# Optimization experiments

Hardware: AMD Instinct MI355X
Metric: run time of the kernel (lower is better)

## Reference

```python
import jax, jax.numpy as jnp
import numpy as np

N = 100000   # nodes
E = 1600000  # edges (before self-loops)
D_IN = 128
HID = 64
H1 = 4       # heads of conv1
OUT = 2
EPS = 1e-5
NEG_SLOPE = 0.2


def setup_inputs():
    key = jax.random.key(0)
    ks = jax.random.split(key, 12)
    s = 0.1
    return {
        "x": jax.random.normal(ks[0], (N, D_IN), jnp.float32),
        "edge_index": jax.random.randint(ks[1], (2, E), 0, N, jnp.int64),
        "W1": jax.random.normal(ks[2], (D_IN, H1 * HID), jnp.float32) * s,
        "att_src1": jax.random.normal(ks[3], (H1, HID), jnp.float32) * s,
        "att_dst1": jax.random.normal(ks[4], (H1, HID), jnp.float32) * s,
        "b1": jnp.zeros((H1 * HID,), jnp.float32),
        "g1": jnp.ones((H1 * HID,), jnp.float32),
        "be1": jnp.zeros((H1 * HID,), jnp.float32),
        "W2": jax.random.normal(ks[5], (H1 * HID, HID), jnp.float32) * s,
        "att_src2": jax.random.normal(ks[6], (1, HID), jnp.float32) * s,
        "att_dst2": jax.random.normal(ks[7], (1, HID), jnp.float32) * s,
        "b2": jnp.zeros((HID,), jnp.float32),
        "g2": jnp.ones((HID,), jnp.float32),
        "be2": jnp.zeros((HID,), jnp.float32),
        "Wc1": jax.random.normal(ks[8], (HID, HID // 2), jnp.float32) * s,
        "bc1": jnp.zeros((HID // 2,), jnp.float32),
        "Wc2": jax.random.normal(ks[9], (HID // 2, OUT), jnp.float32) * s,
        "bc2": jnp.zeros((OUT,), jnp.float32),
    }


def _gat(x, W, a_src, a_dst, bias, src, dst, heads):
    n = x.shape[0]
    h = (x @ W).reshape(n, heads, -1)              # [N,H,C]
    e_src = jnp.einsum('nhc,hc->nh', h, a_src)     # [N,H]
    e_dst = jnp.einsum('nhc,hc->nh', h, a_dst)
    e = jax.nn.leaky_relu(e_src[src] + e_dst[dst], NEG_SLOPE)  # [Etot,H]
    m = jax.ops.segment_max(e, dst, num_segments=n)            # edge-softmax over incoming
    p = jnp.exp(e - m[dst])
    z = jax.ops.segment_sum(p, dst, num_segments=n)
    alpha = p / z[dst]
    msg = alpha[:, :, None] * h[src]               # [Etot,H,C]
    out = jax.ops.segment_sum(msg, dst, num_segments=n)        # [N,H,C]
    return out.reshape(n, -1) + bias               # concat heads + bias


def _bn(x, g, b):
    m = x.mean(0)
    v = x.var(0)
    return g * (x - m) * jax.lax.rsqrt(v + EPS) + b


def reference(x, edge_index, W1, att_src1, att_dst1, b1, g1, be1,
              W2, att_src2, att_dst2, b2, g2, be2, Wc1, bc1, Wc2, bc2):
    n = x.shape[0]
    loops = jnp.arange(n, dtype=edge_index.dtype)
    src = jnp.concatenate([edge_index[0], loops])  # PyG add_self_loops=True
    dst = jnp.concatenate([edge_index[1], loops])

    h = _gat(x, W1, att_src1, att_dst1, b1, src, dst, H1)
    h = jax.nn.elu(_bn(h, g1, be1))                # dropout = identity (eval)
    h = _gat(h, W2, att_src2, att_dst2, b2, src, dst, 1)
    h = jax.nn.elu(_bn(h, g2, be2))
    h = jax.nn.elu(h @ Wc1 + bc1)
    logits = h @ Wc2 + bc2
    return jax.nn.log_softmax(logits, axis=1)
```

## Files before the change

### kernel.cpp

```cpp
#include <hip/hip_runtime.h>
#include <hip/hip_bf16.h>

constexpr int N_  = 100000;
constexpr int E_  = 1600000;
constexpr int PAD = 48;
constexpr int NBKT = 196;
constexpr int BCAP = 16384;

constexpr size_t P_PARAMS = 8192;
constexpr size_t OFF_S1   = 24576;
constexpr size_t OFF_T1   = 25600;
constexpr size_t OFF_S2   = 26624;
constexpr size_t OFF_T2   = 26880;
constexpr size_t OFF_WPK1 = 27136;
constexpr size_t OFF_WPK2 = 92672;
constexpr size_t OFF_DEG  = 125696;
constexpr size_t OFF_ES1  = 525696;
constexpr size_t OFF_ED1  = 2125696;
constexpr size_t OFF_ES2  = 3725696;
constexpr size_t OFF_ED2  = 4125696;
constexpr size_t OFF_CSR  = 4525696;
constexpr size_t OFF_H1   = 23725696;
constexpr size_t OFF_H2   = OFF_H1;
constexpr size_t OFF_AGG2 = OFF_H1 + 12800000;
constexpr size_t OFF_AGG1 = 74925696;
constexpr size_t OFF_BKT  = 126125696;

typedef unsigned short ushortT;
typedef short bf16x8 __attribute__((ext_vector_type(8)));
typedef float f32x4 __attribute__((ext_vector_type(4)));

#define DEV __device__ __forceinline__

DEV float leakyf(float x) { return x > 0.f ? x : 0.2f * x; }
DEV float eluf(float x)   { return x > 0.f ? x : __expf(x) - 1.f; }
DEV float rbf(unsigned short u) { unsigned int b = ((unsigned int)u) << 16; return __uint_as_float(b); }
DEV unsigned short f2b(float f) { __hip_bfloat16 h = __float2bfloat16(f); return *reinterpret_cast<unsigned short*>(&h); }
DEV float sel_head(float4 a, int hd) {
    float r = a.x;
    r = (hd == 1) ? a.y : r;
    r = (hd == 2) ? a.z : r;
    r = (hd == 3) ? a.w : r;
    return r;
}
DEV unsigned short sel_h4(ushort4 u, int hd) {
    unsigned short r = u.x;
    r = (hd == 1) ? u.y : r;
    r = (hd == 2) ? u.z : r;
    r = (hd == 3) ? u.w : r;
    return r;
}
DEV int eread(const int* __restrict__ ei, int mode, int idx) {
    return mode ? ei[(size_t)idx * 2] : ei[idx];
}
DEV unsigned short praw(const void* p, int fm, int idx) {
    return fm ? ((const ushortT*)p)[idx] : f2b(((const float*)p)[idx]);
}

struct CvtArgs { const void* src[14]; int off[15]; };
__global__ __launch_bounds__(256) void k_setup(const void* __restrict__ W1raw, const void* __restrict__ W2raw,
                                               const unsigned int* __restrict__ g1raw, CvtArgs ca,
                                               ushortT* __restrict__ w1, ushortT* __restrict__ w2,
                                               float* __restrict__ pp) {
    int i = blockIdx.x * 256 + threadIdx.x;
    int fm = (g1raw[0] == 0x3F800000u) ? 0 : 1;
    if (i < 32768) {
        int j = i & 7, lane = (i >> 3) & 63, ks = (i >> 9) & 3, ct = i >> 11;
        int src = (ks * 32 + ((lane >> 4) << 3) + j) * 256 + ct * 16 + (lane & 15);
        w1[i] = praw(W1raw, fm, src);
    } else if (i < 49152) {
        int i2 = i - 32768;
        int j = i2 & 7, lane = (i2 >> 3) & 63, ks = (i2 >> 9) & 7, ct = i2 >> 12;
        int src = (ks * 32 + ((lane >> 4) << 3) + j) * 64 + ct * 16 + (lane & 15);
        w2[i2] = praw(W2raw, fm, src);
    } else if (i < 52898) {
        int j = i - 49152;
        int seg = 0;
        #pragma unroll
        for (int s2 = 1; s2 < 14; ++s2) seg += (j >= ca.off[s2]);
        int k = j - ca.off[seg];
        float v;
        if (fm) v = rbf(((const ushortT*)ca.src[seg])[k]);
        else    v = ((const float*)ca.src[seg])[k];
        pp[j] = v;
    }
}

__global__ __launch_bounds__(256) void k_bin(const int* __restrict__ ei,
                                             unsigned int* __restrict__ bucketArr,
                                             int* __restrict__ bucketCursor) {
    __shared__ unsigned int pk[8192];
    __shared__ int sdl[8192];
    __shared__ int ssl[8192];
    __shared__ int cnt[256], scn[256], bse[256], cur[256], gb[256];
    __shared__ int any;
    int tid = threadIdx.x;
    cnt[tid] = 0;
    if (tid == 0) any = 0;
    __syncthreads();
    if (ei[2 * tid + 1] != 0) atomicOr(&any, 1);
    __syncthreads();
    int m = any ? 0 : 1;
    int e0 = blockIdx.x * 8192;
    #pragma unroll 4
    for (int j = 0; j < 32; ++j) {
        int idx = j * 256 + tid;
        int e = e0 + idx;
        if (e < E_) {
            int s = eread(ei, m, e);
            int d = eread(ei, m, E_ + e);
            ssl[idx] = s;
            sdl[idx] = d;
            atomicAdd(&cnt[d >> 9], 1);
        }
    }
    __syncthreads();
    int v = cnt[tid];
    scn[tid] = v;
    __syncthreads();
    for (int d = 1; d < 256; d <<= 1) {
        int t2 = (tid >= d) ? scn[tid - d] : 0;
        __syncthreads();
        scn[tid] += t2;
        __syncthreads();
    }
    int excl = scn[tid] - v;
    bse[tid] = excl;
    cur[tid] = excl;
    __syncthreads();
    #pragma unroll 4
    for (int j = 0; j < 32; ++j) {
        int idx = j * 256 + tid;
        int e = e0 + idx;
        if (e < E_) {
            int s = ssl[idx], d = sdl[idx];
            int b = d >> 9;
            int p = atomicAdd(&cur[b], 1);
            pk[p] = ((unsigned int)(d & 511) << 17) | (unsigned int)s;
        }
    }
    __syncthreads();
    if (tid < NBKT) {
        int c = cnt[tid];
        gb[tid] = (c > 0) ? atomicAdd(&bucketCursor[tid], c) : 0;
    }
    __syncthreads();
    int wv = tid >> 6, ln = tid & 63;
    for (int b = wv; b < NBKT; b += 4) {
        int c = cnt[b];
        int lo = bse[b], g = gb[b];
        for (int i = ln; i < c; i += 64) {
            int gi = g + i;
            if (gi < BCAP) bucketArr[(size_t)b * BCAP + gi] = pk[lo + i];
        }
    }
}

__global__ __launch_bounds__(256) void k_csr(const unsigned int* __restrict__ bucketArr,
                                             const int* __restrict__ bucketCursor,
                                             int* __restrict__ csr, int* __restrict__ deg) {
    __shared__ int dl[512];
    int tid = threadIdx.x;
    int b = blockIdx.x;
    int nbase = b * 512;
    int nb = min(N_ - nbase, 512);
    if (nb <= 0) return;
    dl[tid] = 0; dl[tid + 256] = 0;
    __syncthreads();
    int c = min(bucketCursor[b], BCAP);
    const unsigned int* run = bucketArr + (size_t)b * BCAP;
    for (int i = tid; i < c; i += 256) {
        unsigned int p = run[i];
        int s = (int)(p & 0x1FFFFu);
        int dloc = (int)(p >> 17);
        int slot = atomicAdd(&dl[dloc], 1);
        if (slot < PAD - 1) csr[(size_t)(nbase + dloc) * PAD + slot] = s;
    }
    __syncthreads();
    for (int t = tid; t < nb; t += 256) {
        int n = nbase + t;
        int cd = min(dl[t], PAD - 1);
        csr[(size_t)n * PAD + cd] = n;
        deg[n] = cd + 1;
    }
}

__global__ __launch_bounds__(256) void k_gemm1f(const void* __restrict__ x,
                                                const unsigned int* __restrict__ g1raw,
                                                const ushortT* __restrict__ wpk,
                                                const float* __restrict__ as1, const float* __restrict__ ad1,
                                                ushortT* __restrict__ h1,
                                                float* __restrict__ es1, float* __restrict__ ed1) {
    __shared__ ushortT xs[32][132];
    int tid = threadIdx.x, w = tid >> 6, lane = tid & 63;
    int l15 = lane & 15, l4 = lane >> 4;
    int row0 = blockIdx.x * 32;
    int fm = (g1raw[0] == 0x3F800000u) ? 0 : 1;
    if (fm) {
        const ushortT* xg = (const ushortT*)x + (size_t)row0 * 128;
        for (int i = tid; i < 512; i += 256) {
            int r = i >> 4, cc = (i & 15) * 8;
            ushort4 a = *(const ushort4*)(xg + r * 128 + cc);
            ushort4 b = *(const ushort4*)(xg + r * 128 + cc + 4);
            *(ushort4*)&xs[r][cc]     = a;
            *(ushort4*)&xs[r][cc + 4] = b;
        }
    } else {
        const float* xg = (const float*)x + (size_t)row0 * 128;
        for (int i = tid; i < 512; i += 256) {
            int r = i >> 4, cc = (i & 15) * 8;
            float4 a = *(const float4*)(xg + r * 128 + cc);
            float4 b = *(const float4*)(xg + r * 128 + cc + 4);
            *(ushort4*)&xs[r][cc]     = make_ushort4(f2b(a.x), f2b(a.y), f2b(a.z), f2b(a.w));
            *(ushort4*)&xs[r][cc + 4] = make_ushort4(f2b(b.x), f2b(b.y), f2b(b.z), f2b(b.w));
        }
    }
    __syncthreads();
    bf16x8 A[2][4];
    #pragma unroll
    for (int rt = 0; rt < 2; ++rt)
        #pragma unroll
        for (int ks = 0; ks < 4; ++ks)
            A[rt][ks] = *(const bf16x8*)&xs[rt * 16 + l15][ks * 32 + l4 * 8];
    f32x4 acc[2][4];
    #pragma unroll
    for (int rt = 0; rt < 2; ++rt)
        #pragma unroll
        for (int ct = 0; ct < 4; ++ct) acc[rt][ct] = (f32x4){0.f, 0.f, 0.f, 0.f};
    const bf16x8* wp = (const bf16x8*)wpk;
    #pragma unroll
    for (int ct = 0; ct < 4; ++ct) {
        int ctg = w * 4 + ct;
        bf16x8 B0 = wp[(ctg * 4 + 0) * 64 + lane];
        bf16x8 B1 = wp[(ctg * 4 + 1) * 64 + lane];
        bf16x8 B2 = wp[(ctg * 4 + 2) * 64 + lane];
        bf16x8 B3 = wp[(ctg * 4 + 3) * 64 + lane];
        #pragma unroll
        for (int rt = 0; rt < 2; ++rt) {
            acc[rt][ct] = __builtin_amdgcn_mfma_f32_16x16x32_bf16(A[rt][0], B0, acc[rt][ct], 0, 0, 0);
            acc[rt][ct] = __builtin_amdgcn_mfma_f32_16x16x32_bf16(A[rt][1], B1, acc[rt][ct], 0, 0, 0);
            acc[rt][ct] = __builtin_amdgcn_mfma_f32_16x16x32_bf16(A[rt][2], B2, acc[rt][ct], 0, 0, 0);
            acc[rt][ct] = __builtin_amdgcn_mfma_f32_16x16x32_bf16(A[rt][3], B3, acc[rt][ct], 0, 0, 0);
        }
    }
    float asc[4], adc[4];
    #pragma unroll
    for (int ct = 0; ct < 4; ++ct) {
        asc[ct] = as1[w * 64 + ct * 16 + l15];
        adc[ct] = ad1[w * 64 + ct * 16 + l15];
    }
    float pes[2][4], ped[2][4];
    #pragma unroll
    for (int rt = 0; rt < 2; ++rt)
        #pragma unroll
        for (int r = 0; r < 4; ++r) { pes[rt][r] = 0.f; ped[rt][r] = 0.f; }
    #pragma unroll
    for (int rt = 0; rt < 2; ++rt)
        #pragma unroll
        for (int ct = 0; ct < 4; ++ct)
            #pragma unroll
            for (int r = 0; r < 4; ++r) {
                float v = acc[rt][ct][r];
                int row = row0 + rt * 16 + l4 * 4 + r;
                h1[(size_t)row * 256 + w * 64 + ct * 16 + l15] = f2b(v);
                pes[rt][r] = fmaf(v, asc[ct], pes[rt][r]);
                ped[rt][r] = fmaf(v, adc[ct], ped[rt][r]);
            }
    #pragma unroll
    for (int d = 1; d < 16; d <<= 1)
        #pragma unroll
        for (int rt = 0; rt < 2; ++rt)
            #pragma unroll
            for (int r = 0; r < 4; ++r) {
                pes[rt][r] += __shfl_xor(pes[rt][r], d);
                ped[rt][r] += __shfl_xor(ped[rt][r], d);
            }
    if (l15 == 0) {
        #pragma unroll
        for (int rt = 0; rt < 2; ++rt)
            #pragma unroll
            for (int r = 0; r < 4; ++r) {
                int row = row0 + rt * 16 + l4 * 4 + r;
                es1[row * 4 + w] = pes[rt][r];
                ed1[row * 4 + w] = ped[rt][r];
            }
    }
}

__global__ __launch_bounds__(256) void k_lagg1(const ushortT* __restrict__ h1,
                                               const float* __restrict__ es1, const float* __restrict__ ed1,
                                               const int* __restrict__ deg, const int* __restrict__ csr,
                                               const float* __restrict__ b1, ushortT* __restrict__ out) {
    __shared__ int ssrc[4][PAD];
    __shared__ ushort4 sp[4][PAD];
    int wid = threadIdx.x >> 6;
    int lane = threadIdx.x & 63;
    int n = blockIdx.x * 4 + wid;
    int cnt = deg[n];
    int start = n * PAD;
    float4 ed = ((const float4*)ed1)[n];
    float z0 = 0.f, z1 = 0.f, z2 = 0.f, z3 = 0.f;
    if (lane < cnt) {
        int s = csr[start + lane];
        ssrc[wid][lane] = s;
        float4 es = ((const float4*)es1)[s];
        float p0 = __expf(leakyf(es.x + ed.x));
        float p1 = __expf(leakyf(es.y + ed.y));
        float p2 = __expf(leakyf(es.z + ed.z));
        float p3 = __expf(leakyf(es.w + ed.w));
        sp[wid][lane] = make_ushort4(f2b(p0), f2b(p1), f2b(p2), f2b(p3));
        z0 = p0; z1 = p1; z2 = p2; z3 = p3;
    }
    #pragma unroll
    for (int d = 1; d < 64; d <<= 1) {
        z0 += __shfl_xor(z0, d); z1 += __shfl_xor(z1, d);
        z2 += __shfl_xor(z2, d); z3 += __shfl_xor(z3, d);
    }
    int half = lane >> 5, lh = lane & 31, hd = lh >> 3;
    float izh = sel_head(make_float4(1.f / z0, 1.f / z1, 1.f / z2, 1.f / z3), hd);
    float a0 = 0.f, a1 = 0.f, a2 = 0.f, a3 = 0.f, a4 = 0.f, a5 = 0.f, a6 = 0.f, a7 = 0.f;
    float c0 = 0.f, c1 = 0.f, c2 = 0.f, c3 = 0.f, c4 = 0.f, c5 = 0.f, c6 = 0.f, c7 = 0.f;
    int iters = (cnt + 1) >> 1;
    for (int t = 0; t < iters; t += 4) {
        int i0 = 2 * t + half;
        int i1 = i0 + 2, i2 = i0 + 4, i3 = i0 + 6;
        bool v0 = i0 < cnt, v1 = i1 < cnt, v2 = i2 < cnt, v3 = i3 < cnt;
        int s0 = ssrc[wid][v0 ? i0 : 0];
        int s1 = ssrc[wid][v1 ? i1 : 0];
        int s2 = ssrc[wid][v2 ? i2 : 0];
        int s3 = ssrc[wid][v3 ? i3 : 0];
        ushort4 u0 = sp[wid][v0 ? i0 : 0];
        ushort4 u1 = sp[wid][v1 ? i1 : 0];
        ushort4 u2 = sp[wid][v2 ? i2 : 0];
        ushort4 u3 = sp[wid][v3 ? i3 : 0];
        float w0 = v0 ? rbf(sel_h4(u0, hd)) * izh : 0.f;
        float w1 = v1 ? rbf(sel_h4(u1, hd)) * izh : 0.f;
        float w2 = v2 ? rbf(sel_h4(u2, hd)) * izh : 0.f;
        float w3 = v3 ? rbf(sel_h4(u3, hd)) * izh : 0.f;
        uint4 r0 = *(const uint4*)(h1 + (size_t)s0 * 256 + lh * 8);
        uint4 r1 = *(const uint4*)(h1 + (size_t)s1 * 256 + lh * 8);
        uint4 r2 = *(const uint4*)(h1 + (size_t)s2 * 256 + lh * 8);
        uint4 r3 = *(const uint4*)(h1 + (size_t)s3 * 256 + lh * 8);
        a0 = fmaf(w0, rbf((unsigned short)(r0.x & 0xffff)), a0);
        a1 = fmaf(w0, rbf((unsigned short)(r0.x >> 16)), a1);
        a2 = fmaf(w0, rbf((unsigned short)(r0.y & 0xffff)), a2);
        a3 = fmaf(w0, rbf((unsigned short)(r0.y >> 16)), a3);
        a4 = fmaf(w0, rbf((unsigned short)(r0.z & 0xffff)), a4);
        a5 = fmaf(w0, rbf((unsigned short)(r0.z >> 16)), a5);
        a6 = fmaf(w0, rbf((unsigned short)(r0.w & 0xffff)), a6);
        a7 = fmaf(w0, rbf((unsigned short)(r0.w >> 16)), a7);
        c0 = fmaf(w1, rbf((unsigned short)(r1.x & 0xffff)), c0);
        c1 = fmaf(w1, rbf((unsigned short)(r1.x >> 16)), c1);
        c2 = fmaf(w1, rbf((unsigned short)(r1.y & 0xffff)), c2);
        c3 = fmaf(w1, rbf((unsigned short)(r1.y >> 16)), c3);
        c4 = fmaf(w1, rbf((unsigned short)(r1.z & 0xffff)), c4);
        c5 = fmaf(w1, rbf((unsigned short)(r1.z >> 16)), c5);
        c6 = fmaf(w1, rbf((unsigned short)(r1.w & 0xffff)), c6);
        c7 = fmaf(w1, rbf((unsigned short)(r1.w >> 16)), c7);
        a0 = fmaf(w2, rbf((unsigned short)(r2.x & 0xffff)), a0);
        a1 = fmaf(w2, rbf((unsigned short)(r2.x >> 16)), a1);
        a2 = fmaf(w2, rbf((unsigned short)(r2.y & 0xffff)), a2);
        a3 = fmaf(w2, rbf((unsigned short)(r2.y >> 16)), a3);
        a4 = fmaf(w2, rbf((unsigned short)(r2.z & 0xffff)), a4);
        a5 = fmaf(w2, rbf((unsigned short)(r2.z >> 16)), a5);
        a6 = fmaf(w2, rbf((unsigned short)(r2.w & 0xffff)), a6);
        a7 = fmaf(w2, rbf((unsigned short)(r2.w >> 16)), a7);
        c0 = fmaf(w3, rbf((unsigned short)(r3.x & 0xffff)), c0);
        c1 = fmaf(w3, rbf((unsigned short)(r3.x >> 16)), c1);
        c2 = fmaf(w3, rbf((unsigned short)(r3.y & 0xffff)), c2);
        c3 = fmaf(w3, rbf((unsigned short)(r3.y >> 16)), c3);
        c4 = fmaf(w3, rbf((unsigned short)(r3.z & 0xffff)), c4);
        c5 = fmaf(w3, rbf((unsigned short)(r3.z >> 16)), c5);
        c6 = fmaf(w3, rbf((unsigned short)(r3.w & 0xffff)), c6);
        c7 = fmaf(w3, rbf((unsigned short)(r3.w >> 16)), c7);
    }
    a0 += c0; a1 += c1; a2 += c2; a3 += c3; a4 += c4; a5 += c5; a6 += c6; a7 += c7;
    a0 += __shfl_xor(a0, 32); a1 += __shfl_xor(a1, 32);
    a2 += __shfl_xor(a2, 32); a3 += __shfl_xor(a3, 32);
    a4 += __shfl_xor(a4, 32); a5 += __shfl_xor(a5, 32);
    a6 += __shfl_xor(a6, 32); a7 += __shfl_xor(a7, 32);
    if (half == 0) {
        float4 b0 = *(const float4*)(b1 + lh * 8);
        float4 b1v = *(const float4*)(b1 + lh * 8 + 4);
        ushort4 o0 = make_ushort4(f2b(a0 + b0.x), f2b(a1 + b0.y), f2b(a2 + b0.z), f2b(a3 + b0.w));
        ushort4 o1 = make_ushort4(f2b(a4 + b1v.x), f2b(a5 + b1v.y), f2b(a6 + b1v.z), f2b(a7 + b1v.w));
        *(ushort4*)(out + (size_t)n * 256 + lh * 8)     = o0;
        *(ushort4*)(out + (size_t)n * 256 + lh * 8 + 4) = o1;
    }
}

__global__ __launch_bounds__(256) void k_bnstats1(const ushortT* __restrict__ a, double* __restrict__ sums,
                                                  double* __restrict__ sumsq) {
    __shared__ float lss[256][9], lsq[256][9];
    int tid = threadIdx.x;
    int c8 = tid & 31, rr = tid >> 5;
    int r0 = blockIdx.x * 512;
    int r1 = min(r0 + 512, N_);
    float s[8] = {0, 0, 0, 0, 0, 0, 0, 0}, q[8] = {0, 0, 0, 0, 0, 0, 0, 0};
    for (int r = r0 + rr; r < r1; r += 8) {
        uint4 u = *(const uint4*)(a + (size_t)r * 256 + c8 * 8);
        unsigned int uw[4] = {u.x, u.y, u.z, u.w};
        #pragma unroll
        for (int k = 0; k < 4; ++k) {
            float v0 = rbf((unsigned short)(uw[k] & 0xffff));
            float v1 = rbf((unsigned short)(uw[k] >> 16));
            s[2 * k]     += v0; q[2 * k]     += v0 * v0;
            s[2 * k + 1] += v1; q[2 * k + 1] += v1 * v1;
        }
    }
    #pragma unroll
    for (int k = 0; k < 8; ++k) { lss[tid][k] = s[k]; lsq[tid][k] = q[k]; }
    __syncthreads();
    if (tid < 32) {
        float S[8] = {0, 0, 0, 0, 0, 0, 0, 0}, Q[8] = {0, 0, 0, 0, 0, 0, 0, 0};
        #pragma unroll
        for (int g = 0; g < 8; ++g)
            #pragma unroll
            for (int k = 0; k < 8; ++k) { S[k] += lss[g * 32 + tid][k]; Q[k] += lsq[g * 32 + tid][k]; }
        #pragma unroll
        for (int k = 0; k < 8; ++k) {
            atomicAdd(&sums[tid * 8 + k], (double)S[k]);
            atomicAdd(&sumsq[tid * 8 + k], (double)Q[k]);
        }
    }
}

__global__ void k_bnfin(const double* __restrict__ sums, const double* __restrict__ sumsq,
                        const float* __restrict__ g, const float* __restrict__ be,
                        float* __restrict__ s, float* __restrict__ t, int C) {
    int c = threadIdx.x;
    if (c < C) {
        double mean = sums[c] / (double)N_;
        double var = fmax(sumsq[c] / (double)N_ - mean * mean, 0.0);
        double sc = (double)g[c] / sqrt(var + 1e-5);
        s[c] = (float)sc;
        t[c] = (float)((double)be[c] - mean * sc);
    }
}

__global__ __launch_bounds__(256) void k_gemm2f(const ushortT* __restrict__ agg1,
                                                const ushortT* __restrict__ wpk2,
                                                const float* __restrict__ sc1, const float* __restrict__ tc1,
                                                const float* __restrict__ as2, const float* __restrict__ ad2,
                                                ushortT* __restrict__ h2,
                                                float* __restrict__ es2, float* __restrict__ ed2) {
    int tid = threadIdx.x, w = tid >> 6, lane = tid & 63;
    int l15 = lane & 15, l4 = lane >> 4;
    int row0 = blockIdx.x * 64;
    int arow = row0 + w * 16 + l15;
    int ar = min(arow, N_ - 1);
    bf16x8 A[8];
    #pragma unroll
    for (int ks = 0; ks < 8; ++ks) {
        const ushortT* ap = agg1 + (size_t)ar * 256 + ks * 32 + l4 * 8;
        int pi = ks * 32 + l4 * 8;
        uint4 u = *(const uint4*)ap;
        float4 s0 = *(const float4*)(sc1 + pi);
        float4 s1 = *(const float4*)(sc1 + pi + 4);
        float4 t0 = *(const float4*)(tc1 + pi);
        float4 t1 = *(const float4*)(tc1 + pi + 4);
        float e0 = eluf(fmaf(rbf((unsigned short)(u.x & 0xffff)), s0.x, t0.x));
        float e1 = eluf(fmaf(rbf((unsigned short)(u.x >> 16)),    s0.y, t0.y));
        float e2 = eluf(fmaf(rbf((unsigned short)(u.y & 0xffff)), s0.z, t0.z));
        float e3 = eluf(fmaf(rbf((unsigned short)(u.y >> 16)),    s0.w, t0.w));
        float e4 = eluf(fmaf(rbf((unsigned short)(u.z & 0xffff)), s1.x, t1.x));
        float e5 = eluf(fmaf(rbf((unsigned short)(u.z >> 16)),    s1.y, t1.y));
        float e6 = eluf(fmaf(rbf((unsigned short)(u.w & 0xffff)), s1.z, t1.z));
        float e7 = eluf(fmaf(rbf((unsigned short)(u.w >> 16)),    s1.w, t1.w));
        A[ks] = (bf16x8){(short)f2b(e0), (short)f2b(e1), (short)f2b(e2), (short)f2b(e3),
                         (short)f2b(e4), (short)f2b(e5), (short)f2b(e6), (short)f2b(e7)};
    }
    f32x4 acc[4];
    #pragma unroll
    for (int ct = 0; ct < 4; ++ct) acc[ct] = (f32x4){0.f, 0.f, 0.f, 0.f};
    const bf16x8* wp = (const bf16x8*)wpk2;
    #pragma unroll
    for (int ct = 0; ct < 4; ++ct) {
        #pragma unroll
        for (int ks = 0; ks < 8; ++ks) {
            bf16x8 B = wp[(ct * 8 + ks) * 64 + lane];
            acc[ct] = __builtin_amdgcn_mfma_f32_16x16x32_bf16(A[ks], B, acc[ct], 0, 0, 0);
        }
    }
    float asc[4], adc[4];
    #pragma unroll
    for (int ct = 0; ct < 4; ++ct) {
        asc[ct] = as2[ct * 16 + l15];
        adc[ct] = ad2[ct * 16 + l15];
    }
    float pes[4] = {0.f, 0.f, 0.f, 0.f}, ped[4] = {0.f, 0.f, 0.f, 0.f};
    #pragma unroll
    for (int ct = 0; ct < 4; ++ct)
        #pragma unroll
        for (int r = 0; r < 4; ++r) {
            float v = acc[ct][r];
            int row = row0 + w * 16 + l4 * 4 + r;
            if (row < N_) h2[(size_t)row * 64 + ct * 16 + l15] = f2b(v);
            pes[r] = fmaf(v, asc[ct], pes[r]);
            ped[r] = fmaf(v, adc[ct], ped[r]);
        }
    #pragma unroll
    for (int d = 1; d < 16; d <<= 1)
        #pragma unroll
        for (int r = 0; r < 4; ++r) {
            pes[r] += __shfl_xor(pes[r], d);
            ped[r] += __shfl_xor(ped[r], d);
        }
    if (l15 == 0) {
        #pragma unroll
        for (int r = 0; r < 4; ++r) {
            int row = row0 + w * 16 + l4 * 4 + r;
            if (row < N_) { es2[row] = pes[r]; ed2[row] = ped[r]; }
        }
    }
}

__global__ __launch_bounds__(256) void k_lagg2(const ushortT* __restrict__ h2,
                                               const float* __restrict__ es2, const float* __restrict__ ed2,
                                               const int* __restrict__ deg, const int* __restrict__ csr,
                                               const float* __restrict__ b2, float* __restrict__ out) {
    __shared__ int ssrc[4][PAD];
    __shared__ float sp[4][PAD];
    int wid = threadIdx.x >> 6;
    int lane = threadIdx.x & 63;
    int n = blockIdx.x * 4 + wid;
    int cnt = deg[n];
    int start = n * PAD;
    float ed = ed2[n];
    float z = 0.f;
    if (lane < cnt) {
        int s = csr[start + lane];
        ssrc[wid][lane] = s;
        float p = __expf(leakyf(es2[s] + ed));
        sp[wid][lane] = p;
        z = p;
    }
    #pragma unroll
    for (int d = 1; d < 64; d <<= 1) z += __shfl_xor(z, d);
    float iz = 1.f / z;
    int half = lane >> 5, lh = lane & 31;
    float a0 = 0.f, a1 = 0.f, c0 = 0.f, c1 = 0.f;
    int iters = (cnt + 1) >> 1;
    for (int t = 0; t < iters; t += 4) {
        int i0 = 2 * t + half;
        int i1 = i0 + 2, i2 = i0 + 4, i3 = i0 + 6;
        bool v0 = i0 < cnt, v1 = i1 < cnt, v2 = i2 < cnt, v3 = i3 < cnt;
        int s0 = ssrc[wid][v0 ? i0 : 0];
        int s1 = ssrc[wid][v1 ? i1 : 0];
        int s2 = ssrc[wid][v2 ? i2 : 0];
        int s3 = ssrc[wid][v3 ? i3 : 0];
        float w0 = v0 ? sp[wid][i0] * iz : 0.f;
        float w1 = v1 ? sp[wid][i1] * iz : 0.f;
        float w2 = v2 ? sp[wid][i2] * iz : 0.f;
        float w3 = v3 ? sp[wid][i3] * iz : 0.f;
        unsigned int u0 = *(const unsigned int*)(h2 + (size_t)s0 * 64 + lh * 2);
        unsigned int u1 = *(const unsigned int*)(h2 + (size_t)s1 * 64 + lh * 2);
        unsigned int u2 = *(const unsigned int*)(h2 + (size_t)s2 * 64 + lh * 2);
        unsigned int u3 = *(const unsigned int*)(h2 + (size_t)s3 * 64 + lh * 2);
        a0 = fmaf(w0, rbf((unsigned short)(u0 & 0xffff)), a0);
        a1 = fmaf(w0, rbf((unsigned short)(u0 >> 16)), a1);
        c0 = fmaf(w1, rbf((unsigned short)(u1 & 0xffff)), c0);
        c1 = fmaf(w1, rbf((unsigned short)(u1 >> 16)), c1);
        a0 = fmaf(w2, rbf((unsigned short)(u2 & 0xffff)), a0);
        a1 = fmaf(w2, rbf((unsigned short)(u2 >> 16)), a1);
        c0 = fmaf(w3, rbf((unsigned short)(u3 & 0xffff)), c0);
        c1 = fmaf(w3, rbf((unsigned short)(u3 >> 16)), c1);
    }
    a0 += c0; a1 += c1;
    a0 += __shfl_xor(a0, 32);
    a1 += __shfl_xor(a1, 32);
    if (half == 0) {
        out[(size_t)n * 64 + lh * 2 + 0] = a0 + b2[lh * 2 + 0];
        out[(size_t)n * 64 + lh * 2 + 1] = a1 + b2[lh * 2 + 1];
    }
}

__global__ __launch_bounds__(256) void k_bnstats2(const float* __restrict__ a, double* __restrict__ sums,
                                                  double* __restrict__ sumsq) {
    __shared__ double sm[256], sq[256];
    int tid = threadIdx.x;
    int c = tid & 63, rr = tid >> 6;
    int r0 = blockIdx.x * 1024;
    int r1 = min(r0 + 1024, N_);
    double s = 0.0, q = 0.0;
    for (int r = r0 + rr; r < r1; r += 4) { float v = a[(size_t)r * 64 + c]; s += v; q += (double)v * v; }
    sm[tid] = s; sq[tid] = q; __syncthreads();
    if (tid < 64) {
        s = sm[tid] + sm[tid + 64] + sm[tid + 128] + sm[tid + 192];
        q = sq[tid] + sq[tid + 64] + sq[tid + 128] + sq[tid + 192];
        atomicAdd(&sums[tid], s);
        atomicAdd(&sumsq[tid], q);
    }
}

__global__ __launch_bounds__(256) void k_cls(const float* __restrict__ agg2, const float* __restrict__ Wc1,
                                             const float* __restrict__ bc1, const float* __restrict__ Wc2,
                                             const float* __restrict__ bc2, const float* __restrict__ s2,
                                             const float* __restrict__ t2, float* __restrict__ out) {
    __shared__ float w1s[2048];
    __shared__ float w2s[64];
    __shared__ float b1s[32];
    __shared__ float b2s[2];
    __shared__ float ss[64], ts[64];
    int tid = threadIdx.x;
    for (int i = tid; i < 2048; i += 256) w1s[i] = Wc1[i];
    if (tid < 64) { w2s[tid] = Wc2[tid]; ss[tid] = s2[tid]; ts[tid] = t2[tid]; }
    if (tid < 32) b1s[tid] = bc1[tid];
    if (tid < 2)  b2s[tid] = bc2[tid];
    __syncthreads();
    int n = blockIdx.x * 256 + tid;
    if (n >= N_) return;
    float hv[64];
    const float4* rp = (const float4*)(agg2 + (size_t)n * 64);
    #pragma unroll
    for (int q = 0; q < 16; ++q) {
        float4 v = rp[q];
        float tmp[4] = {v.x, v.y, v.z, v.w};
        #pragma unroll
        for (int c4 = 0; c4 < 4; ++c4) {
            int c = q * 4 + c4;
            hv[c] = eluf(fmaf(tmp[c4], ss[c], ts[c]));
        }
    }
    float l0 = b2s[0], l1 = b2s[1];
    for (int j = 0; j < 32; ++j) {
        float a = b1s[j];
        #pragma unroll
        for (int k = 0; k < 64; ++k) a = fmaf(hv[k], w1s[k * 32 + j], a);
        float u = eluf(a);
        l0 = fmaf(u, w2s[j * 2 + 0], l0);
        l1 = fmaf(u, w2s[j * 2 + 1], l1);
    }
    float mx = fmaxf(l0, l1);
    float lse = mx + __logf(__expf(l0 - mx) + __expf(l1 - mx));
    out[(size_t)n * 2 + 0] = l0 - lse;
    out[(size_t)n * 2 + 1] = l1 - lse;
}

extern "C" void kernel_launch(void* const* d_in, const int* in_sizes, int n_in,
                              void* d_out, int out_size, void* d_ws, size_t ws_size,
                              hipStream_t stream) {
    float* out = (float*)d_out;

    char* ws = (char*)d_ws;
    double* sums1  = (double*)(ws + 0);
    double* sumsq1 = (double*)(ws + 2048);
    double* sums2  = (double*)(ws + 4096);
    double* sumsq2 = (double*)(ws + 4608);
    int* bcur = (int*)(ws + 5120);
    float* s1 = (float*)(ws + OFF_S1), *t1 = (float*)(ws + OFF_T1);
    float* s2 = (float*)(ws + OFF_S2), *t2 = (float*)(ws + OFF_T2);

    float* pp   = (float*)(ws + P_PARAMS);
    float* as1f = pp + 0;
    float* ad1f = pp + 256;
    float* b1f  = pp + 512;
    float* g1f  = pp + 768;
    float* be1f = pp + 1024;
    float* as2f = pp + 1280;
    float* ad2f = pp + 1344;
    float* b2f  = pp + 1408;
    float* g2f  = pp + 1472;
    float* be2f = pp + 1536;
    float* Wc1f = pp + 1600;
    float* bc1f = pp + 3648;
    float* Wc2f = pp + 3680;
    float* bc2f = pp + 3744;

    ushortT* wpk1 = (ushortT*)(ws + OFF_WPK1);
    ushortT* wpk2 = (ushortT*)(ws + OFF_WPK2);
    int* deg    = (int*)(ws + OFF_DEG);
    int* csr    = (int*)(ws + OFF_CSR);
    float* es1  = (float*)(ws + OFF_ES1);
    float* ed1  = (float*)(ws + OFF_ED1);
    float* es2  = (float*)(ws + OFF_ES2);
    float* ed2  = (float*)(ws + OFF_ED2);
    ushortT* h1 = (ushortT*)(ws + OFF_H1);
    ushortT* h2 = (ushortT*)(ws + OFF_H2);
    float* agg2 = (float*)(ws + OFF_AGG2);
    ushortT* agg1 = (ushortT*)(ws + OFF_AGG1);
    unsigned int* bkt = (unsigned int*)(ws + OFF_BKT);

    hipMemsetAsync(ws, 0, 6144, stream);

    CvtArgs ca;
    const int srcIdx[14] = {3, 4, 5, 6, 7, 9, 10, 11, 12, 13, 14, 15, 16, 17};
    const int offsEl[15] = {0, 256, 512, 768, 1024, 1280, 1344, 1408, 1472, 1536, 1600, 3648, 3680, 3744, 3746};
    for (int i = 0; i < 14; ++i) ca.src[i] = d_in[srcIdx[i]];
    for (int i = 0; i < 15; ++i) ca.off[i] = offsEl[i];
    k_setup<<<207, 256, 0, stream>>>(d_in[2], d_in[8], (const unsigned int*)d_in[6], ca, wpk1, wpk2, pp);

    k_bin<<<(E_ + 8191) / 8192, 256, 0, stream>>>((const int*)d_in[1], bkt, bcur);
    k_csr<<<NBKT, 256, 0, stream>>>(bkt, bcur, csr, deg);

    k_gemm1f<<<N_ / 32, 256, 0, stream>>>(d_in[0], (const unsigned int*)d_in[6], wpk1, as1f, ad1f, h1, es1, ed1);
    k_lagg1<<<N_ / 4, 256, 0, stream>>>(h1, es1, ed1, deg, csr, b1f, agg1);
    k_bnstats1<<<196, 256, 0, stream>>>(agg1, sums1, sumsq1);
    k_bnfin<<<1, 256, 0, stream>>>(sums1, sumsq1, g1f, be1f, s1, t1, 256);

    k_gemm2f<<<(N_ + 63) / 64, 256, 0, stream>>>(agg1, wpk2, s1, t1, as2f, ad2f, h2, es2, ed2);
    k_lagg2<<<N_ / 4, 256, 0, stream>>>(h2, es2, ed2, deg, csr, b2f, agg2);
    k_bnstats2<<<98, 256, 0, stream>>>(agg2, sums2, sumsq2);
    k_bnfin<<<1, 64, 0, stream>>>(sums2, sumsq2, g2f, be2f, s2, t2, 64);

    k_cls<<<(N_ + 255) / 256, 256, 0, stream>>>(agg2, Wc1f, bc1f, Wc2f, bc2f, s2, t2, out);
}
```

Measured before the change: 451.7 us.

## Fold BN finalize into consumers, bf16 agg2, zero workspace in setup

Removes the two single-block BN-finalize kernels: each block of k_gemm2f and k_cls now recomputes per-channel scale and shift from the double sums into shared memory. The hipMemsetAsync is replaced by zeroing inside k_setup, which is launched with extra blocks for that purpose. Layer-2 aggregation output is stored as bf16 instead of fp32, halving the traffic read by the BN stats and classifier kernels. Together these cut three launches and some memory traffic, at the cost of redundant per-block double-precision work and lower precision in the agg2 path.

```diff
diff --git a/kernel.cpp b/kernel.cpp
--- a/kernel.cpp
+++ b/kernel.cpp
@@ -8,10 +8,6 @@
 constexpr int BCAP = 16384;
 
 constexpr size_t P_PARAMS = 8192;
-constexpr size_t OFF_S1   = 24576;
-constexpr size_t OFF_T1   = 25600;
-constexpr size_t OFF_S2   = 26624;
-constexpr size_t OFF_T2   = 26880;
 constexpr size_t OFF_WPK1 = 27136;
 constexpr size_t OFF_WPK2 = 92672;
 constexpr size_t OFF_DEG  = 125696;
@@ -61,7 +57,7 @@
 __global__ __launch_bounds__(256) void k_setup(const void* __restrict__ W1raw, const void* __restrict__ W2raw,
                                                const unsigned int* __restrict__ g1raw, CvtArgs ca,
                                                ushortT* __restrict__ w1, ushortT* __restrict__ w2,
-                                               float* __restrict__ pp) {
+                                               float* __restrict__ pp, unsigned int* __restrict__ zbase) {
     int i = blockIdx.x * 256 + threadIdx.x;
     int fm = (g1raw[0] == 0x3F800000u) ? 0 : 1;
     if (i < 32768) {
@@ -83,6 +79,8 @@
         if (fm) v = rbf(((const ushortT*)ca.src[seg])[k]);
         else    v = ((const float*)ca.src[seg])[k];
         pp[j] = v;
+    } else if (i >= 52992 && i < 54528) {
+        zbase[i - 52992] = 0u;
     }
 }
 
@@ -425,26 +423,23 @@
     }
 }
 
-__global__ void k_bnfin(const double* __restrict__ sums, const double* __restrict__ sumsq,
-                        const float* __restrict__ g, const float* __restrict__ be,
-                        float* __restrict__ s, float* __restrict__ t, int C) {
-    int c = threadIdx.x;
-    if (c < C) {
-        double mean = sums[c] / (double)N_;
-        double var = fmax(sumsq[c] / (double)N_ - mean * mean, 0.0);
-        double sc = (double)g[c] / sqrt(var + 1e-5);
-        s[c] = (float)sc;
-        t[c] = (float)((double)be[c] - mean * sc);
-    }
-}
-
 __global__ __launch_bounds__(256) void k_gemm2f(const ushortT* __restrict__ agg1,
                                                 const ushortT* __restrict__ wpk2,
-                                                const float* __restrict__ sc1, const float* __restrict__ tc1,
+                                                const double* __restrict__ sums1, const double* __restrict__ sumsq1,
+                                                const float* __restrict__ g1, const float* __restrict__ be1,
                                                 const float* __restrict__ as2, const float* __restrict__ ad2,
                                                 ushortT* __restrict__ h2,
                                                 float* __restrict__ es2, float* __restrict__ ed2) {
+    __shared__ float ssS[256], ttS[256];
     int tid = threadIdx.x, w = tid >> 6, lane = tid & 63;
+    {
+        double mean = sums1[tid] / (double)N_;
+        double var = fmax(sumsq1[tid] / (double)N_ - mean * mean, 0.0);
+        double sc = (double)g1[tid] / sqrt(var + 1e-5);
+        ssS[tid] = (float)sc;
+        ttS[tid] = (float)((double)be1[tid] - mean * sc);
+    }
+    __syncthreads();
     int l15 = lane & 15, l4 = lane >> 4;
     int row0 = blockIdx.x * 64;
     int arow = row0 + w * 16 + l15;
@@ -455,10 +450,10 @@
         const ushortT* ap = agg1 + (size_t)ar * 256 + ks * 32 + l4 * 8;
         int pi = ks * 32 + l4 * 8;
         uint4 u = *(const uint4*)ap;
-        float4 s0 = *(const float4*)(sc1 + pi);
-        float4 s1 = *(const float4*)(sc1 + pi + 4);
-        float4 t0 = *(const float4*)(tc1 + pi);
-        float4 t1 = *(const float4*)(tc1 + pi + 4);
+        float4 s0 = *(const float4*)(ssS + pi);
+        float4 s1 = *(const float4*)(ssS + pi + 4);
+        float4 t0 = *(const float4*)(ttS + pi);
+        float4 t1 = *(const float4*)(ttS + pi + 4);
         float e0 = eluf(fmaf(rbf((unsigned short)(u.x & 0xffff)), s0.x, t0.x));
         float e1 = eluf(fmaf(rbf((unsigned short)(u.x >> 16)),    s0.y, t0.y));
         float e2 = eluf(fmaf(rbf((unsigned short)(u.y & 0xffff)), s0.z, t0.z));
@@ -518,7 +513,7 @@
 __global__ __launch_bounds__(256) void k_lagg2(const ushortT* __restrict__ h2,
                                                const float* __restrict__ es2, const float* __restrict__ ed2,
                                                const int* __restrict__ deg, const int* __restrict__ csr,
-                                               const float* __restrict__ b2, float* __restrict__ out) {
+                                               const float* __restrict__ b2, ushortT* __restrict__ out) {
     __shared__ int ssrc[4][PAD];
     __shared__ float sp[4][PAD];
     int wid = threadIdx.x >> 6;
@@ -570,12 +565,12 @@
     a0 += __shfl_xor(a0, 32);
     a1 += __shfl_xor(a1, 32);
     if (half == 0) {
-        out[(size_t)n * 64 + lh * 2 + 0] = a0 + b2[lh * 2 + 0];
-        out[(size_t)n * 64 + lh * 2 + 1] = a1 + b2[lh * 2 + 1];
-    }
-}
-
-__global__ __launch_bounds__(256) void k_bnstats2(const float* __restrict__ a, double* __restrict__ sums,
+        ushort2 o = make_ushort2(f2b(a0 + b2[lh * 2 + 0]), f2b(a1 + b2[lh * 2 + 1]));
+        *(ushort2*)(out + (size_t)n * 64 + lh * 2) = o;
+    }
+}
+
+__global__ __launch_bounds__(256) void k_bnstats2(const ushortT* __restrict__ a, double* __restrict__ sums,
                                                   double* __restrict__ sumsq) {
     __shared__ double sm[256], sq[256];
     int tid = threadIdx.x;
@@ -583,7 +578,7 @@
     int r0 = blockIdx.x * 1024;
     int r1 = min(r0 + 1024, N_);
     double s = 0.0, q = 0.0;
-    for (int r = r0 + rr; r < r1; r += 4) { float v = a[(size_t)r * 64 + c]; s += v; q += (double)v * v; }
+    for (int r = r0 + rr; r < r1; r += 4) { float v = rbf(a[(size_t)r * 64 + c]); s += v; q += (double)v * v; }
     sm[tid] = s; sq[tid] = q; __syncthreads();
     if (tid < 64) {
         s = sm[tid] + sm[tid + 64] + sm[tid + 128] + sm[tid + 192];
@@ -593,10 +588,12 @@
     }
 }
 
-__global__ __launch_bounds__(256) void k_cls(const float* __restrict__ agg2, const float* __restrict__ Wc1,
+__global__ __launch_bounds__(256) void k_cls(const ushortT* __restrict__ agg2, const float* __restrict__ Wc1,
                                              const float* __restrict__ bc1, const float* __restrict__ Wc2,
-                                             const float* __restrict__ bc2, const float* __restrict__ s2,
-                                             const float* __restrict__ t2, float* __restrict__ out) {
+                                             const float* __restrict__ bc2,
+                                             const double* __restrict__ sums2, const double* __restrict__ sumsq2,
+                                             const float* __restrict__ g2, const float* __restrict__ be2,
+                                             float* __restrict__ out) {
     __shared__ float w1s[2048];
     __shared__ float w2s[64];
     __shared__ float b1s[32];
@@ -604,22 +601,30 @@
     __shared__ float ss[64], ts[64];
     int tid = threadIdx.x;
     for (int i = tid; i < 2048; i += 256) w1s[i] = Wc1[i];
-    if (tid < 64) { w2s[tid] = Wc2[tid]; ss[tid] = s2[tid]; ts[tid] = t2[tid]; }
+    if (tid < 64) {
+        w2s[tid] = Wc2[tid];
+        double mean = sums2[tid] / (double)N_;
+        double var = fmax(sumsq2[tid] / (double)N_ - mean * mean, 0.0);
+        double sc = (double)g2[tid] / sqrt(var + 1e-5);
+        ss[tid] = (float)sc;
+        ts[tid] = (float)((double)be2[tid] - mean * sc);
+    }
     if (tid < 32) b1s[tid] = bc1[tid];
     if (tid < 2)  b2s[tid] = bc2[tid];
     __syncthreads();
     int n = blockIdx.x * 256 + tid;
     if (n >= N_) return;
     float hv[64];
-    const float4* rp = (const float4*)(agg2 + (size_t)n * 64);
-    #pragma unroll
-    for (int q = 0; q < 16; ++q) {
-        float4 v = rp[q];
-        float tmp[4] = {v.x, v.y, v.z, v.w};
-        #pragma unroll
-        for (int c4 = 0; c4 < 4; ++c4) {
-            int c = q * 4 + c4;
-            hv[c] = eluf(fmaf(tmp[c4], ss[c], ts[c]));
+    const uint4* rp = (const uint4*)(agg2 + (size_t)n * 64);
+    #pragma unroll
+    for (int q = 0; q < 8; ++q) {
+        uint4 u = rp[q];
+        unsigned int uw[4] = {u.x, u.y, u.z, u.w};
+        #pragma unroll
+        for (int k = 0; k < 4; ++k) {
+            int c = q * 8 + k * 2;
+            hv[c]     = eluf(fmaf(rbf((unsigned short)(uw[k] & 0xffff)), ss[c], ts[c]));
+            hv[c + 1] = eluf(fmaf(rbf((unsigned short)(uw[k] >> 16)), ss[c + 1], ts[c + 1]));
         }
     }
     float l0 = b2s[0], l1 = b2s[1];
@@ -648,8 +653,6 @@
     double* sums2  = (double*)(ws + 4096);
     double* sumsq2 = (double*)(ws + 4608);
     int* bcur = (int*)(ws + 5120);
-    float* s1 = (float*)(ws + OFF_S1), *t1 = (float*)(ws + OFF_T1);
-    float* s2 = (float*)(ws + OFF_S2), *t2 = (float*)(ws + OFF_T2);
 
     float* pp   = (float*)(ws + P_PARAMS);
     float* as1f = pp + 0;
@@ -677,18 +680,17 @@
     float* ed2  = (float*)(ws + OFF_ED2);
     ushortT* h1 = (ushortT*)(ws + OFF_H1);
     ushortT* h2 = (ushortT*)(ws + OFF_H2);
-    float* agg2 = (float*)(ws + OFF_AGG2);
+    ushortT* agg2 = (ushortT*)(ws + OFF_AGG2);
     ushortT* agg1 = (ushortT*)(ws + OFF_AGG1);
     unsigned int* bkt = (unsigned int*)(ws + OFF_BKT);
-
-    hipMemsetAsync(ws, 0, 6144, stream);
 
     CvtArgs ca;
     const int srcIdx[14] = {3, 4, 5, 6, 7, 9, 10, 11, 12, 13, 14, 15, 16, 17};
     const int offsEl[15] = {0, 256, 512, 768, 1024, 1280, 1344, 1408, 1472, 1536, 1600, 3648, 3680, 3744, 3746};
     for (int i = 0; i < 14; ++i) ca.src[i] = d_in[srcIdx[i]];
     for (int i = 0; i < 15; ++i) ca.off[i] = offsEl[i];
-    k_setup<<<207, 256, 0, stream>>>(d_in[2], d_in[8], (const unsigned int*)d_in[6], ca, wpk1, wpk2, pp);
+    k_setup<<<214, 256, 0, stream>>>(d_in[2], d_in[8], (const unsigned int*)d_in[6], ca,
+                                     wpk1, wpk2, pp, (unsigned int*)ws);
 
     k_bin<<<(E_ + 8191) / 8192, 256, 0, stream>>>((const int*)d_in[1], bkt, bcur);
     k_csr<<<NBKT, 256, 0, stream>>>(bkt, bcur, csr, deg);
@@ -696,12 +698,12 @@
     k_gemm1f<<<N_ / 32, 256, 0, stream>>>(d_in[0], (const unsigned int*)d_in[6], wpk1, as1f, ad1f, h1, es1, ed1);
     k_lagg1<<<N_ / 4, 256, 0, stream>>>(h1, es1, ed1, deg, csr, b1f, agg1);
     k_bnstats1<<<196, 256, 0, stream>>>(agg1, sums1, sumsq1);
-    k_bnfin<<<1, 256, 0, stream>>>(sums1, sumsq1, g1f, be1f, s1, t1, 256);
-
-    k_gemm2f<<<(N_ + 63) / 64, 256, 0, stream>>>(agg1, wpk2, s1, t1, as2f, ad2f, h2, es2, ed2);
+
+    k_gemm2f<<<(N_ + 63) / 64, 256, 0, stream>>>(agg1, wpk2, sums1, sumsq1, g1f, be1f,
+                                                 as2f, ad2f, h2, es2, ed2);
     k_lagg2<<<N_ / 4, 256, 0, stream>>>(h2, es2, ed2, deg, csr, b2f, agg2);
     k_bnstats2<<<98, 256, 0, stream>>>(agg2, sums2, sumsq2);
-    k_bnfin<<<1, 64, 0, stream>>>(sums2, sumsq2, g2f, be2f, s2, t2, 64);
-
-    k_cls<<<(N_ + 255) / 256, 256, 0, stream>>>(agg2, Wc1f, bc1f, Wc2f, bc2f, s2, t2, out);
-}
+
+    k_cls<<<(N_ + 255) / 256, 256, 0, stream>>>(agg2, Wc1f, bc1f, Wc2f, bc2f,
+                                                sums2, sumsq2, g2f, be2f, out);
+}
```

Measured after the change: 434.4 us. 3.8% less time.
